# Kernel tuning notes

Hardware: AMD Instinct MI355X
Metric: run time of the kernel (lower is better)

The kernel has to match this reference:

```python
import jax, jax.numpy as jnp
import numpy as np

B, F_SIZE, DIM = 2048, 32, 64
LAYER_SIZES = (128, 128)


def setup_inputs() -> dict:
    key = jax.random.key(0)
    k1, k2, k3 = jax.random.split(key, 3)
    inputs = jax.random.normal(k1, (B, F_SIZE, DIM), dtype=jnp.float32)
    # Conv1d(kernel=1) weights: (out_channels, in_channels)
    W0 = jax.random.normal(k2, (128, F_SIZE * F_SIZE), dtype=jnp.float32) * 0.03
    b0 = jnp.zeros((128,), dtype=jnp.float32)
    # split_half -> field_nums[1] = 64 -> in_channels = 64 * 32 = 2048
    W1 = jax.random.normal(k3, (128, 64 * F_SIZE), dtype=jnp.float32) * 0.03
    b1 = jnp.zeros((128,), dtype=jnp.float32)
    return {"inputs": inputs, "W0": W0, "b0": b0, "W1": W1, "b1": b1}


def _cin_forward(inputs, Ws, bs):
    batch, _, dim = inputs.shape
    x0 = inputs
    h = inputs
    finals = []
    n_layers = len(Ws)
    for i in range(n_layers):
        H = h.shape[1]
        M = x0.shape[1]
        # outer-product interaction: (b, H, M, d) -> (b, H*M, d)
        z = jnp.einsum('bhd,bmd->bhmd', h, x0).reshape(batch, H * M, dim)
        # 1x1 conv == per-position channel matmul
        out = jnp.einsum('bcd,oc->bod', z, Ws[i]) + bs[i][None, :, None]
        out = jax.nn.relu(out)
        size = Ws[i].shape[0]
        if i != n_layers - 1:
            # split_half: first half feeds next layer, second half is output
            h = out[:, : size // 2, :]
            finals.append(out[:, size // 2 :, :])
        else:
            finals.append(out)
    result = jnp.concatenate(finals, axis=1)  # (b, 64 + 128, d)
    return jnp.sum(result, axis=-1)           # (b, 192)


def reference(inputs, W0, b0, W1, b1):
    return _cin_forward(inputs, (W0, W1), (b0, b1))
```

## Files before the change

### kernel.cpp

```cpp
#include <hip/hip_runtime.h>


#define BATCH 2048
#define FSZ   32
#define DIM   64
#define K0    1024
#define K1    2048
#define OUTC  192

#define W0_ELEMS (128 * K0)
#define W1_ELEMS (128 * K1)
#define TOT_ELEMS (W0_ELEMS + W1_ELEMS)
#define CVT_THREADS (TOT_ELEMS / 4)

typedef _Float16 v8h __attribute__((ext_vector_type(8)));
typedef float    v4f __attribute__((ext_vector_type(4)));

#define XT_PITCH 40
#define XD_PITCH 66
#define HD_PITCH 66

__global__ void convert_w_kernel(const float* __restrict__ W0,
                                 const float* __restrict__ W1,
                                 _Float16* __restrict__ wsw) {
    int t = blockIdx.x * blockDim.x + threadIdx.x;
    if (t >= CVT_THREADS) return;
    int e = t * 4;
    const float* src;
    _Float16* dst;
    if (e < W0_ELEMS) {
        int j0 = e & 7, lane = (e >> 3) & 63, s = (e >> 9) & 7, ks = e >> 12;
        src = W0 + (size_t)(s * 16 + (lane & 15)) * K0
                 + ks * 32 + (lane >> 4) * 8 + j0;
        dst = wsw + e;
    } else {
        int u = e - W0_ELEMS;
        int j0 = u & 7, lane = (u >> 3) & 63, s = (u >> 9) & 7, ks = u >> 12;
        src = W1 + (size_t)(s * 16 + (lane & 15)) * K1
                 + ks * 32 + (lane >> 4) * 8 + j0;
        dst = wsw + W0_ELEMS + u;
    }
    float4 v = *(const float4*)src;
    dst[0] = (_Float16)v.x;
    dst[1] = (_Float16)v.y;
    dst[2] = (_Float16)v.z;
    dst[3] = (_Float16)v.w;
}

__global__ __launch_bounds__(256, 4) void cin_kernel(
    const float* __restrict__ X,
    const float* __restrict__ b0,
    const float* __restrict__ b1,
    const _Float16* __restrict__ Wsw,
    float* __restrict__ out)
{
    __shared__ _Float16 xT[2][DIM * XT_PITCH];
    __shared__ _Float16 xD[2][FSZ * XD_PITCH];
    __shared__ _Float16 h1D[2][64 * HD_PITCH];

    const int b0i  = blockIdx.x * 2;
    const int tid  = threadIdx.x;
    const int wave = tid >> 6;
    const int lane = tid & 63;
    const int p    = wave & 1;
    const int rh   = wave >> 1;
    const int quad = lane >> 4;
    const int col  = lane & 15;

    #pragma unroll
    for (int i = tid; i < 2 * FSZ * DIM / 4; i += 256) {
        int pp = i >> 9, r4 = i & 511;
        float4 v = *(const float4*)(X + (size_t)(b0i + pp) * (FSZ * DIM) + r4 * 4);
        int m = (r4 * 4) >> 6, d = (r4 * 4) & 63;
        _Float16 f0 = (_Float16)v.x, f1 = (_Float16)v.y,
                 f2 = (_Float16)v.z, f3 = (_Float16)v.w;
        xT[pp][(d + 0) * XT_PITCH + m] = f0;
        xT[pp][(d + 1) * XT_PITCH + m] = f1;
        xT[pp][(d + 2) * XT_PITCH + m] = f2;
        xT[pp][(d + 3) * XT_PITCH + m] = f3;
        xD[pp][m * XD_PITCH + d + 0] = f0;
        xD[pp][m * XD_PITCH + d + 1] = f1;
        xD[pp][m * XD_PITCH + d + 2] = f2;
        xD[pp][m * XD_PITCH + d + 3] = f3;
    }
    __syncthreads();

    v8h xv8[4];
    int dd[4];
    #pragma unroll
    for (int t = 0; t < 4; ++t) {
        dd[t] = 16 * t + col;
        xv8[t] = *(const v8h*)(&xT[p][dd[t] * XT_PITCH + quad * 8]);
    }

    v4f acc[4][4];
    #pragma unroll
    for (int f = 0; f < 4; ++f)
        #pragma unroll
        for (int t = 0; t < 4; ++t) acc[f][t] = (v4f)0.0f;

    {
        const _Float16* Wk = Wsw + (size_t)(rh * 4) * 512 + (size_t)lane * 8;
        #pragma unroll 2
        for (int ks = 0; ks < 32; ++ks) {
            v8h a0 = *(const v8h*)(Wk);
            v8h a1 = *(const v8h*)(Wk + 512);
            v8h a2 = *(const v8h*)(Wk + 1024);
            v8h a3 = *(const v8h*)(Wk + 1536);
            Wk += 4096;
            #pragma unroll
            for (int t = 0; t < 4; ++t) {
                _Float16 s = xD[p][ks * XD_PITCH + dd[t]];
                v8h s8 = {s, s, s, s, s, s, s, s};
                v8h bfr = s8 * xv8[t];
                acc[0][t] = __builtin_amdgcn_mfma_f32_16x16x32_f16(a0, bfr, acc[0][t], 0, 0, 0);
                acc[1][t] = __builtin_amdgcn_mfma_f32_16x16x32_f16(a1, bfr, acc[1][t], 0, 0, 0);
                acc[2][t] = __builtin_amdgcn_mfma_f32_16x16x32_f16(a2, bfr, acc[2][t], 0, 0, 0);
                acc[3][t] = __builtin_amdgcn_mfma_f32_16x16x32_f16(a3, bfr, acc[3][t], 0, 0, 0);
            }
        }
    }

    if (rh == 0) {
        #pragma unroll
        for (int f = 0; f < 4; ++f) {
            #pragma unroll
            for (int reg = 0; reg < 4; ++reg) {
                const int o = f * 16 + quad * 4 + reg;
                const float bias = b0[o];
                #pragma unroll
                for (int t = 0; t < 4; ++t) {
                    float v = acc[f][t][reg] + bias;
                    v = v > 0.0f ? v : 0.0f;
                    h1D[p][o * HD_PITCH + dd[t]] = (_Float16)v;
                }
            }
        }
    } else {
        #pragma unroll
        for (int f = 0; f < 4; ++f) {
            #pragma unroll
            for (int reg = 0; reg < 4; ++reg) {
                const int o = 64 + f * 16 + quad * 4 + reg;
                const float bias = b0[o];
                float s = 0.0f;
                #pragma unroll
                for (int t = 0; t < 4; ++t) {
                    float v = acc[f][t][reg] + bias;
                    s += (v > 0.0f ? v : 0.0f);
                }
                s += __shfl_xor(s, 1);
                s += __shfl_xor(s, 2);
                s += __shfl_xor(s, 4);
                s += __shfl_xor(s, 8);
                if (col == 0) out[(size_t)(b0i + p) * OUTC + (o - 64)] = s;
            }
        }
    }
    __syncthreads();

    #pragma unroll
    for (int f = 0; f < 4; ++f)
        #pragma unroll
        for (int t = 0; t < 4; ++t) acc[f][t] = (v4f)0.0f;

    {
        const _Float16* Wk = Wsw + W0_ELEMS + (size_t)(rh * 4) * 512 + (size_t)lane * 8;
        #pragma unroll 2
        for (int ks = 0; ks < 64; ++ks) {
            v8h a0 = *(const v8h*)(Wk);
            v8h a1 = *(const v8h*)(Wk + 512);
            v8h a2 = *(const v8h*)(Wk + 1024);
            v8h a3 = *(const v8h*)(Wk + 1536);
            Wk += 4096;
            #pragma unroll
            for (int t = 0; t < 4; ++t) {
                _Float16 s = h1D[p][ks * HD_PITCH + dd[t]];
                v8h s8 = {s, s, s, s, s, s, s, s};
                v8h bfr = s8 * xv8[t];
                acc[0][t] = __builtin_amdgcn_mfma_f32_16x16x32_f16(a0, bfr, acc[0][t], 0, 0, 0);
                acc[1][t] = __builtin_amdgcn_mfma_f32_16x16x32_f16(a1, bfr, acc[1][t], 0, 0, 0);
                acc[2][t] = __builtin_amdgcn_mfma_f32_16x16x32_f16(a2, bfr, acc[2][t], 0, 0, 0);
                acc[3][t] = __builtin_amdgcn_mfma_f32_16x16x32_f16(a3, bfr, acc[3][t], 0, 0, 0);
            }
        }
    }

    #pragma unroll
    for (int f = 0; f < 4; ++f) {
        #pragma unroll
        for (int reg = 0; reg < 4; ++reg) {
            const int o = rh * 64 + f * 16 + quad * 4 + reg;
            const float bias = b1[o];
            float s = 0.0f;
            #pragma unroll
            for (int t = 0; t < 4; ++t) {
                float v = acc[f][t][reg] + bias;
                s += (v > 0.0f ? v : 0.0f);
            }
            s += __shfl_xor(s, 1);
            s += __shfl_xor(s, 2);
            s += __shfl_xor(s, 4);
            s += __shfl_xor(s, 8);
            if (col == 0) out[(size_t)(b0i + p) * OUTC + 64 + o] = s;
        }
    }
}

extern "C" void kernel_launch(void* const* d_in, const int* in_sizes, int n_in,
                              void* d_out, int out_size, void* d_ws, size_t ws_size,
                              hipStream_t stream) {
    const float* X  = (const float*)d_in[0];
    const float* W0 = (const float*)d_in[1];
    const float* b0 = (const float*)d_in[2];
    const float* W1 = (const float*)d_in[3];
    const float* b1 = (const float*)d_in[4];
    float* out = (float*)d_out;
    _Float16* wsw = (_Float16*)d_ws;

    convert_w_kernel<<<(CVT_THREADS + 255) / 256, 256, 0, stream>>>(W0, W1, wsw);
    cin_kernel<<<BATCH / 2, 256, 0, stream>>>(X, b0, b1, wsw, out);
}
```

Before: 150.1 us.

## Prefetch next weight fragments and pack LDS scalars into vector loads

Adds register double-buffering of the weight A-fragments and the per-step LDS scalars in both MFMA loops, so the global loads for step k+1 are issued before the MFMAs of step k. Reorders the x and h1 LDS layouts so the four per-lane scalars for each step sit contiguously and load as one 8-byte read instead of four 2-byte reads, and packs the h1 stores the same way. The cost is higher register pressure from holding two sets of A-fragments, which could reduce occupancy under launch_bounds(256,4). The wrap-around prefetch on the last iteration also does a redundant load.

```diff
diff --git a/kernel.cpp b/kernel.cpp
--- a/kernel.cpp
+++ b/kernel.cpp
@@ -14,11 +14,10 @@
 #define CVT_THREADS (TOT_ELEMS / 4)
 
 typedef _Float16 v8h __attribute__((ext_vector_type(8)));
+typedef _Float16 v4h __attribute__((ext_vector_type(4)));
 typedef float    v4f __attribute__((ext_vector_type(4)));
 
 #define XT_PITCH 40
-#define XD_PITCH 66
-#define HD_PITCH 66
 
 __global__ void convert_w_kernel(const float* __restrict__ W0,
                                  const float* __restrict__ W1,
@@ -55,8 +54,8 @@
     float* __restrict__ out)
 {
     __shared__ _Float16 xT[2][DIM * XT_PITCH];
-    __shared__ _Float16 xD[2][FSZ * XD_PITCH];
-    __shared__ _Float16 h1D[2][64 * HD_PITCH];
+    __shared__ _Float16 xS[2][FSZ * 64];
+    __shared__ _Float16 h1S[2][64 * 64];
 
     const int b0i  = blockIdx.x * 2;
     const int tid  = threadIdx.x;
@@ -68,30 +67,29 @@
     const int col  = lane & 15;
 
     #pragma unroll
-    for (int i = tid; i < 2 * FSZ * DIM / 4; i += 256) {
-        int pp = i >> 9, r4 = i & 511;
+    for (int i = 0; i < 4; ++i) {
+        int idx = tid + i * 256;
+        int pp = idx >> 9, r4 = idx & 511;
         float4 v = *(const float4*)(X + (size_t)(b0i + pp) * (FSZ * DIM) + r4 * 4);
         int m = (r4 * 4) >> 6, d = (r4 * 4) & 63;
+        int tq = d >> 4, c = d & 15;
         _Float16 f0 = (_Float16)v.x, f1 = (_Float16)v.y,
                  f2 = (_Float16)v.z, f3 = (_Float16)v.w;
         xT[pp][(d + 0) * XT_PITCH + m] = f0;
         xT[pp][(d + 1) * XT_PITCH + m] = f1;
         xT[pp][(d + 2) * XT_PITCH + m] = f2;
         xT[pp][(d + 3) * XT_PITCH + m] = f3;
-        xD[pp][m * XD_PITCH + d + 0] = f0;
-        xD[pp][m * XD_PITCH + d + 1] = f1;
-        xD[pp][m * XD_PITCH + d + 2] = f2;
-        xD[pp][m * XD_PITCH + d + 3] = f3;
+        xS[pp][m * 64 + (c + 0) * 4 + tq] = f0;
+        xS[pp][m * 64 + (c + 1) * 4 + tq] = f1;
+        xS[pp][m * 64 + (c + 2) * 4 + tq] = f2;
+        xS[pp][m * 64 + (c + 3) * 4 + tq] = f3;
     }
     __syncthreads();
 
     v8h xv8[4];
-    int dd[4];
-    #pragma unroll
-    for (int t = 0; t < 4; ++t) {
-        dd[t] = 16 * t + col;
-        xv8[t] = *(const v8h*)(&xT[p][dd[t] * XT_PITCH + quad * 8]);
-    }
+    #pragma unroll
+    for (int t = 0; t < 4; ++t)
+        xv8[t] = *(const v8h*)(&xT[p][(16 * t + col) * XT_PITCH + quad * 8]);
 
     v4f acc[4][4];
     #pragma unroll
@@ -100,24 +98,32 @@
         for (int t = 0; t < 4; ++t) acc[f][t] = (v4f)0.0f;
 
     {
-        const _Float16* Wk = Wsw + (size_t)(rh * 4) * 512 + (size_t)lane * 8;
+        const _Float16* Wb = Wsw + (size_t)(rh * 4) * 512 + (size_t)lane * 8;
+        v8h aC[4], aN[4];
+        v4h svC, svN;
+        #pragma unroll
+        for (int i = 0; i < 4; ++i) aC[i] = *(const v8h*)(Wb + i * 512);
+        svC = *(const v4h*)(&xS[p][col * 4]);
         #pragma unroll 2
         for (int ks = 0; ks < 32; ++ks) {
-            v8h a0 = *(const v8h*)(Wk);
-            v8h a1 = *(const v8h*)(Wk + 512);
-            v8h a2 = *(const v8h*)(Wk + 1024);
-            v8h a3 = *(const v8h*)(Wk + 1536);
-            Wk += 4096;
+            const int kn = (ks + 1) & 31;
+            const _Float16* Wn = Wb + (size_t)kn * 4096;
+            #pragma unroll
+            for (int i = 0; i < 4; ++i) aN[i] = *(const v8h*)(Wn + i * 512);
+            svN = *(const v4h*)(&xS[p][kn * 64 + col * 4]);
             #pragma unroll
             for (int t = 0; t < 4; ++t) {
-                _Float16 s = xD[p][ks * XD_PITCH + dd[t]];
+                _Float16 s = svC[t];
                 v8h s8 = {s, s, s, s, s, s, s, s};
                 v8h bfr = s8 * xv8[t];
-                acc[0][t] = __builtin_amdgcn_mfma_f32_16x16x32_f16(a0, bfr, acc[0][t], 0, 0, 0);
-                acc[1][t] = __builtin_amdgcn_mfma_f32_16x16x32_f16(a1, bfr, acc[1][t], 0, 0, 0);
-                acc[2][t] = __builtin_amdgcn_mfma_f32_16x16x32_f16(a2, bfr, acc[2][t], 0, 0, 0);
-                acc[3][t] = __builtin_amdgcn_mfma_f32_16x16x32_f16(a3, bfr, acc[3][t], 0, 0, 0);
-            }
+                acc[0][t] = __builtin_amdgcn_mfma_f32_16x16x32_f16(aC[0], bfr, acc[0][t], 0, 0, 0);
+                acc[1][t] = __builtin_amdgcn_mfma_f32_16x16x32_f16(aC[1], bfr, acc[1][t], 0, 0, 0);
+                acc[2][t] = __builtin_amdgcn_mfma_f32_16x16x32_f16(aC[2], bfr, acc[2][t], 0, 0, 0);
+                acc[3][t] = __builtin_amdgcn_mfma_f32_16x16x32_f16(aC[3], bfr, acc[3][t], 0, 0, 0);
+            }
+            #pragma unroll
+            for (int i = 0; i < 4; ++i) aC[i] = aN[i];
+            svC = svN;
         }
     }
 
@@ -128,12 +134,14 @@
             for (int reg = 0; reg < 4; ++reg) {
                 const int o = f * 16 + quad * 4 + reg;
                 const float bias = b0[o];
+                v4h pk;
                 #pragma unroll
                 for (int t = 0; t < 4; ++t) {
                     float v = acc[f][t][reg] + bias;
                     v = v > 0.0f ? v : 0.0f;
-                    h1D[p][o * HD_PITCH + dd[t]] = (_Float16)v;
+                    pk[t] = (_Float16)v;
                 }
+                *(v4h*)(&h1S[p][o * 64 + col * 4]) = pk;
             }
         }
     } else {
@@ -165,24 +173,32 @@
         for (int t = 0; t < 4; ++t) acc[f][t] = (v4f)0.0f;
 
     {
-        const _Float16* Wk = Wsw + W0_ELEMS + (size_t)(rh * 4) * 512 + (size_t)lane * 8;
+        const _Float16* Wb = Wsw + W0_ELEMS + (size_t)(rh * 4) * 512 + (size_t)lane * 8;
+        v8h aC[4], aN[4];
+        v4h svC, svN;
+        #pragma unroll
+        for (int i = 0; i < 4; ++i) aC[i] = *(const v8h*)(Wb + i * 512);
+        svC = *(const v4h*)(&h1S[p][col * 4]);
         #pragma unroll 2
         for (int ks = 0; ks < 64; ++ks) {
-            v8h a0 = *(const v8h*)(Wk);
-            v8h a1 = *(const v8h*)(Wk + 512);
-            v8h a2 = *(const v8h*)(Wk + 1024);
-            v8h a3 = *(const v8h*)(Wk + 1536);
-            Wk += 4096;
+            const int kn = (ks + 1) & 63;
+            const _Float16* Wn = Wb + (size_t)kn * 4096;
+            #pragma unroll
+            for (int i = 0; i < 4; ++i) aN[i] = *(const v8h*)(Wn + i * 512);
+            svN = *(const v4h*)(&h1S[p][kn * 64 + col * 4]);
             #pragma unroll
             for (int t = 0; t < 4; ++t) {
-                _Float16 s = h1D[p][ks * HD_PITCH + dd[t]];
+                _Float16 s = svC[t];
                 v8h s8 = {s, s, s, s, s, s, s, s};
                 v8h bfr = s8 * xv8[t];
-                acc[0][t] = __builtin_amdgcn_mfma_f32_16x16x32_f16(a0, bfr, acc[0][t], 0, 0, 0);
-                acc[1][t] = __builtin_amdgcn_mfma_f32_16x16x32_f16(a1, bfr, acc[1][t], 0, 0, 0);
-                acc[2][t] = __builtin_amdgcn_mfma_f32_16x16x32_f16(a2, bfr, acc[2][t], 0, 0, 0);
-                acc[3][t] = __builtin_amdgcn_mfma_f32_16x16x32_f16(a3, bfr, acc[3][t], 0, 0, 0);
-            }
+                acc[0][t] = __builtin_amdgcn_mfma_f32_16x16x32_f16(aC[0], bfr, acc[0][t], 0, 0, 0);
+                acc[1][t] = __builtin_amdgcn_mfma_f32_16x16x32_f16(aC[1], bfr, acc[1][t], 0, 0, 0);
+                acc[2][t] = __builtin_amdgcn_mfma_f32_16x16x32_f16(aC[2], bfr, acc[2][t], 0, 0, 0);
+                acc[3][t] = __builtin_amdgcn_mfma_f32_16x16x32_f16(aC[3], bfr, acc[3][t], 0, 0, 0);
+            }
+            #pragma unroll
+            for (int i = 0; i < 4; ++i) aC[i] = aN[i];
+            svC = svN;
         }
     }
 
```

After: 148.7 us. About the same (-1.0%).

## Stage weights into LDS with double-buffered async loads, four batches per block

Applied to the files above, without the earlier changes.

Each block now handles four batch rows with 512 threads. Weight fragments are staged cooperatively into a double-buffered LDS tile using global_load_lds and shared across the four batch rows, instead of every wave loading weights from global memory on its own. The x and h1 scalar operands are also re-laid out so one vector LDS read feeds all four t-tiles. The cost is a block-wide barrier on every k-step and more LDS per block, which may limit occupancy. Correctness also depends on the async LDS loads having landed by the time the barrier is reached.

```diff
diff --git a/kernel.cpp b/kernel.cpp
--- a/kernel.cpp
+++ b/kernel.cpp
@@ -14,11 +14,10 @@
 #define CVT_THREADS (TOT_ELEMS / 4)
 
 typedef _Float16 v8h __attribute__((ext_vector_type(8)));
+typedef _Float16 v4h __attribute__((ext_vector_type(4)));
 typedef float    v4f __attribute__((ext_vector_type(4)));
 
 #define XT_PITCH 40
-#define XD_PITCH 66
-#define HD_PITCH 66
 
 __global__ void convert_w_kernel(const float* __restrict__ W0,
                                  const float* __restrict__ W1,
@@ -47,51 +46,63 @@
     dst[3] = (_Float16)v.w;
 }
 
-__global__ __launch_bounds__(256, 4) void cin_kernel(
+__device__ __forceinline__ void stage_w(const _Float16* gsrc, _Float16* ldst) {
+    __builtin_amdgcn_global_load_lds(
+        (const __attribute__((address_space(1))) void*)gsrc,
+        (__attribute__((address_space(3))) void*)ldst,
+        16, 0, 0);
+}
+
+__global__ __launch_bounds__(512, 4) void cin_kernel(
     const float* __restrict__ X,
     const float* __restrict__ b0,
     const float* __restrict__ b1,
     const _Float16* __restrict__ Wsw,
     float* __restrict__ out)
 {
-    __shared__ _Float16 xT[2][DIM * XT_PITCH];
-    __shared__ _Float16 xD[2][FSZ * XD_PITCH];
-    __shared__ _Float16 h1D[2][64 * HD_PITCH];
-
-    const int b0i  = blockIdx.x * 2;
+    __shared__ _Float16 wbuf[2][4096];
+    __shared__ _Float16 xmem[18432];
+
+    _Float16* const xT  = xmem;
+    _Float16* const xS  = xmem + 10240;
+    _Float16* const h1S = xmem;
+
     const int tid  = threadIdx.x;
     const int wave = tid >> 6;
     const int lane = tid & 63;
-    const int p    = wave & 1;
-    const int rh   = wave >> 1;
+    const int p    = wave & 3;
+    const int rh   = wave >> 2;
     const int quad = lane >> 4;
     const int col  = lane & 15;
-
-    #pragma unroll
-    for (int i = tid; i < 2 * FSZ * DIM / 4; i += 256) {
-        int pp = i >> 9, r4 = i & 511;
+    const int b0i  = blockIdx.x * 4;
+
+    #pragma unroll
+    for (int i = 0; i < 4; ++i) {
+        int idx = tid + i * 512;
+        int pp = idx >> 9, r4 = idx & 511;
         float4 v = *(const float4*)(X + (size_t)(b0i + pp) * (FSZ * DIM) + r4 * 4);
         int m = (r4 * 4) >> 6, d = (r4 * 4) & 63;
+        int tq = d >> 4, cc = d & 15;
         _Float16 f0 = (_Float16)v.x, f1 = (_Float16)v.y,
                  f2 = (_Float16)v.z, f3 = (_Float16)v.w;
-        xT[pp][(d + 0) * XT_PITCH + m] = f0;
-        xT[pp][(d + 1) * XT_PITCH + m] = f1;
-        xT[pp][(d + 2) * XT_PITCH + m] = f2;
-        xT[pp][(d + 3) * XT_PITCH + m] = f3;
-        xD[pp][m * XD_PITCH + d + 0] = f0;
-        xD[pp][m * XD_PITCH + d + 1] = f1;
-        xD[pp][m * XD_PITCH + d + 2] = f2;
-        xD[pp][m * XD_PITCH + d + 3] = f3;
-    }
+        _Float16* xTp = xT + pp * 2560;
+        _Float16* xSp = xS + pp * 2048;
+        xTp[(d + 0) * XT_PITCH + m] = f0;
+        xTp[(d + 1) * XT_PITCH + m] = f1;
+        xTp[(d + 2) * XT_PITCH + m] = f2;
+        xTp[(d + 3) * XT_PITCH + m] = f3;
+        xSp[m * 64 + (cc + 0) * 4 + tq] = f0;
+        xSp[m * 64 + (cc + 1) * 4 + tq] = f1;
+        xSp[m * 64 + (cc + 2) * 4 + tq] = f2;
+        xSp[m * 64 + (cc + 3) * 4 + tq] = f3;
+    }
+    stage_w(Wsw + (size_t)wave * 512 + lane * 8, &wbuf[0][wave * 512]);
     __syncthreads();
 
     v8h xv8[4];
-    int dd[4];
-    #pragma unroll
-    for (int t = 0; t < 4; ++t) {
-        dd[t] = 16 * t + col;
-        xv8[t] = *(const v8h*)(&xT[p][dd[t] * XT_PITCH + quad * 8]);
-    }
+    #pragma unroll
+    for (int t = 0; t < 4; ++t)
+        xv8[t] = *(const v8h*)(xT + p * 2560 + (16 * t + col) * XT_PITCH + quad * 8);
 
     v4f acc[4][4];
     #pragma unroll
@@ -99,26 +110,30 @@
         #pragma unroll
         for (int t = 0; t < 4; ++t) acc[f][t] = (v4f)0.0f;
 
-    {
-        const _Float16* Wk = Wsw + (size_t)(rh * 4) * 512 + (size_t)lane * 8;
-        #pragma unroll 2
-        for (int ks = 0; ks < 32; ++ks) {
-            v8h a0 = *(const v8h*)(Wk);
-            v8h a1 = *(const v8h*)(Wk + 512);
-            v8h a2 = *(const v8h*)(Wk + 1024);
-            v8h a3 = *(const v8h*)(Wk + 1536);
-            Wk += 4096;
-            #pragma unroll
-            for (int t = 0; t < 4; ++t) {
-                _Float16 s = xD[p][ks * XD_PITCH + dd[t]];
-                v8h s8 = {s, s, s, s, s, s, s, s};
-                v8h bfr = s8 * xv8[t];
-                acc[0][t] = __builtin_amdgcn_mfma_f32_16x16x32_f16(a0, bfr, acc[0][t], 0, 0, 0);
-                acc[1][t] = __builtin_amdgcn_mfma_f32_16x16x32_f16(a1, bfr, acc[1][t], 0, 0, 0);
-                acc[2][t] = __builtin_amdgcn_mfma_f32_16x16x32_f16(a2, bfr, acc[2][t], 0, 0, 0);
-                acc[3][t] = __builtin_amdgcn_mfma_f32_16x16x32_f16(a3, bfr, acc[3][t], 0, 0, 0);
-            }
-        }
+    const int fragOff = rh * 2048 + lane * 8;
+    int c = 0;
+    for (int ks = 0; ks < 32; ++ks) {
+        const size_t nxt = (ks < 31) ? (size_t)(ks + 1) * 4096 : (size_t)W0_ELEMS;
+        stage_w(Wsw + nxt + wave * 512 + lane * 8, &wbuf[c ^ 1][wave * 512]);
+
+        v4h sv = *(const v4h*)(xS + p * 2048 + ks * 64 + col * 4);
+        const _Float16* wb = &wbuf[c][fragOff];
+        v8h a0 = *(const v8h*)(wb);
+        v8h a1 = *(const v8h*)(wb + 512);
+        v8h a2 = *(const v8h*)(wb + 1024);
+        v8h a3 = *(const v8h*)(wb + 1536);
+        #pragma unroll
+        for (int t = 0; t < 4; ++t) {
+            _Float16 s = sv[t];
+            v8h s8 = {s, s, s, s, s, s, s, s};
+            v8h bfr = s8 * xv8[t];
+            acc[0][t] = __builtin_amdgcn_mfma_f32_16x16x32_f16(a0, bfr, acc[0][t], 0, 0, 0);
+            acc[1][t] = __builtin_amdgcn_mfma_f32_16x16x32_f16(a1, bfr, acc[1][t], 0, 0, 0);
+            acc[2][t] = __builtin_amdgcn_mfma_f32_16x16x32_f16(a2, bfr, acc[2][t], 0, 0, 0);
+            acc[3][t] = __builtin_amdgcn_mfma_f32_16x16x32_f16(a3, bfr, acc[3][t], 0, 0, 0);
+        }
+        __syncthreads();
+        c ^= 1;
     }
 
     if (rh == 0) {
@@ -128,12 +143,14 @@
             for (int reg = 0; reg < 4; ++reg) {
                 const int o = f * 16 + quad * 4 + reg;
                 const float bias = b0[o];
+                v4h pk;
                 #pragma unroll
                 for (int t = 0; t < 4; ++t) {
                     float v = acc[f][t][reg] + bias;
                     v = v > 0.0f ? v : 0.0f;
-                    h1D[p][o * HD_PITCH + dd[t]] = (_Float16)v;
+                    pk[t] = (_Float16)v;
                 }
+                *(v4h*)(h1S + p * 4096 + o * 64 + col * 4) = pk;
             }
         }
     } else {
@@ -164,26 +181,29 @@
         #pragma unroll
         for (int t = 0; t < 4; ++t) acc[f][t] = (v4f)0.0f;
 
-    {
-        const _Float16* Wk = Wsw + W0_ELEMS + (size_t)(rh * 4) * 512 + (size_t)lane * 8;
-        #pragma unroll 2
-        for (int ks = 0; ks < 64; ++ks) {
-            v8h a0 = *(const v8h*)(Wk);
-            v8h a1 = *(const v8h*)(Wk + 512);
-            v8h a2 = *(const v8h*)(Wk + 1024);
-            v8h a3 = *(const v8h*)(Wk + 1536);
-            Wk += 4096;
-            #pragma unroll
-            for (int t = 0; t < 4; ++t) {
-                _Float16 s = h1D[p][ks * HD_PITCH + dd[t]];
-                v8h s8 = {s, s, s, s, s, s, s, s};
-                v8h bfr = s8 * xv8[t];
-                acc[0][t] = __builtin_amdgcn_mfma_f32_16x16x32_f16(a0, bfr, acc[0][t], 0, 0, 0);
-                acc[1][t] = __builtin_amdgcn_mfma_f32_16x16x32_f16(a1, bfr, acc[1][t], 0, 0, 0);
-                acc[2][t] = __builtin_amdgcn_mfma_f32_16x16x32_f16(a2, bfr, acc[2][t], 0, 0, 0);
-                acc[3][t] = __builtin_amdgcn_mfma_f32_16x16x32_f16(a3, bfr, acc[3][t], 0, 0, 0);
-            }
-        }
+    for (int ks = 0; ks < 64; ++ks) {
+        if (ks < 63)
+            stage_w(Wsw + (size_t)W0_ELEMS + (size_t)(ks + 1) * 4096 + wave * 512 + lane * 8,
+                    &wbuf[c ^ 1][wave * 512]);
+
+        v4h sv = *(const v4h*)(h1S + p * 4096 + ks * 64 + col * 4);
+        const _Float16* wb = &wbuf[c][fragOff];
+        v8h a0 = *(const v8h*)(wb);
+        v8h a1 = *(const v8h*)(wb + 512);
+        v8h a2 = *(const v8h*)(wb + 1024);
+        v8h a3 = *(const v8h*)(wb + 1536);
+        #pragma unroll
+        for (int t = 0; t < 4; ++t) {
+            _Float16 s = sv[t];
+            v8h s8 = {s, s, s, s, s, s, s, s};
+            v8h bfr = s8 * xv8[t];
+            acc[0][t] = __builtin_amdgcn_mfma_f32_16x16x32_f16(a0, bfr, acc[0][t], 0, 0, 0);
+            acc[1][t] = __builtin_amdgcn_mfma_f32_16x16x32_f16(a1, bfr, acc[1][t], 0, 0, 0);
+            acc[2][t] = __builtin_amdgcn_mfma_f32_16x16x32_f16(a2, bfr, acc[2][t], 0, 0, 0);
+            acc[3][t] = __builtin_amdgcn_mfma_f32_16x16x32_f16(a3, bfr, acc[3][t], 0, 0, 0);
+        }
+        __syncthreads();
+        c ^= 1;
     }
 
     #pragma unroll
@@ -219,5 +239,5 @@
     _Float16* wsw = (_Float16*)d_ws;
 
     convert_w_kernel<<<(CVT_THREADS + 255) / 256, 256, 0, stream>>>(W0, W1, wsw);
-    cin_kernel<<<BATCH / 2, 256, 0, stream>>>(X, b0, b1, wsw, out);
-}
+    cin_kernel<<<BATCH / 4, 512, 0, stream>>>(X, b0, b1, wsw, out);
+}
```

Result: faster. 147.1 us (-2.0%).
